# Kernel tuning notes

Hardware: AMD Instinct MI355X
Metric: run time of the kernel (lower is better)

Reference implementation:

```python
import jax, jax.numpy as jnp
import numpy as np

DIM = 1024
ATT_DIM = 1024
NUM_HEADS = 16
HEAD_DIM = ATT_DIM // NUM_HEADS


def setup_inputs() -> dict:
    key = jax.random.key(0)
    ks = jax.random.split(key, 13)
    s = lambda fan_in: 1.0 / np.sqrt(fan_in)
    bsz, n = 8, 1024
    x = jax.random.normal(ks[0], (bsz, n, DIM), dtype=jnp.float32)
    # Linear weights stored as [in, out] (apply via x @ W + b)
    Wq = jax.random.uniform(ks[1], (DIM, ATT_DIM), minval=-s(DIM), maxval=s(DIM))
    bq = jax.random.uniform(ks[2], (ATT_DIM,), minval=-s(DIM), maxval=s(DIM))
    Wk = jax.random.uniform(ks[3], (DIM, ATT_DIM), minval=-s(DIM), maxval=s(DIM))
    bk = jax.random.uniform(ks[4], (ATT_DIM,), minval=-s(DIM), maxval=s(DIM))
    Wv = jax.random.uniform(ks[5], (DIM, ATT_DIM), minval=-s(DIM), maxval=s(DIM))
    bv = jax.random.uniform(ks[6], (ATT_DIM,), minval=-s(DIM), maxval=s(DIM))
    Win = jax.random.uniform(ks[7], (DIM, HEAD_DIM), minval=-s(DIM), maxval=s(DIM))
    bin_ = jax.random.uniform(ks[8], (HEAD_DIM,), minval=-s(DIM), maxval=s(DIM))
    d_in1 = HEAD_DIM * (NUM_HEADS + 1)
    W1 = jax.random.uniform(ks[9], (d_in1, 2 * DIM), minval=-s(d_in1), maxval=s(d_in1))
    b1 = jax.random.uniform(ks[10], (2 * DIM,), minval=-s(d_in1), maxval=s(d_in1))
    W2 = jax.random.uniform(ks[11], (2 * DIM, DIM), minval=-s(2 * DIM), maxval=s(2 * DIM))
    b2 = jax.random.uniform(ks[12], (DIM,), minval=-s(2 * DIM), maxval=s(2 * DIM))
    return {"x": x, "Wq": Wq, "bq": bq, "Wk": Wk, "bk": bk, "Wv": Wv, "bv": bv,
            "Win": Win, "bin_": bin_, "W1": W1, "b1": b1, "W2": W2, "b2": b2}


def reference(x, Wq, bq, Wk, bk, Wv, bv, Win, bin_, W1, b1, W2, b2):
    bsz, n, _ = x.shape
    scaling = HEAD_DIM ** (-0.5)
    # [b, n, h, d]
    q = (x @ Wq + bq).reshape(bsz, n, NUM_HEADS, HEAD_DIM) * scaling
    k = (x @ Wk + bk).reshape(bsz, n, NUM_HEADS, HEAD_DIM)
    v = (x @ Wv + bv).reshape(bsz, n, NUM_HEADS, HEAD_DIM)
    # scores [b, h, n, n]
    score = jnp.einsum('bihd,bjhd->bhij', q, k)
    diag = jnp.eye(n, dtype=bool)  # self positions masked with -inf
    score = jnp.where(diag[None, None], -jnp.inf, score)
    attn = jax.nn.softmax(score, axis=-1)
    out = jnp.einsum('bhij,bjhd->bihd', attn, v).reshape(bsz, n, NUM_HEADS * HEAD_DIM)
    in_ = (x @ Win + bin_)  # [b, n, head_dim]
    out = jnp.concatenate([out, in_], axis=-1)
    h = jax.nn.relu(out @ W1 + b1)
    return h @ W2 + b2
```

## Files before the change

kernel.cpp:

```cpp
#include <hip/hip_runtime.h>

typedef __bf16 bf16;
typedef __attribute__((ext_vector_type(8))) __bf16 bf16x8;
typedef __attribute__((ext_vector_type(4))) __bf16 bf16x4;
typedef __attribute__((ext_vector_type(4))) short short4_t;
typedef __attribute__((ext_vector_type(4))) float floatx4;

typedef const void __attribute__((address_space(1)))* gas1p;
typedef void __attribute__((address_space(3)))* las3p;

#define LOG2E 1.44269504088896340736f

static constexpr int D_MODEL = 1024;
static constexpr int N_HEADS = 16;
static constexpr int HDIM    = 64;
static constexpr int BSZ     = 8;
static constexpr int SEQ     = 1024;
static constexpr int ROWS    = BSZ * SEQ;
static constexpr int FF_IN   = 1088;
static constexpr int FF_HID  = 2048;
static constexpr int QKV_LD  = 3072;

__device__ __forceinline__ floatx4 mfma_bf16(bf16x8 a, bf16x8 b, floatx4 c) {
  return __builtin_amdgcn_mfma_f32_16x16x32_bf16(a, b, c, 0, 0, 0);
}

__device__ __forceinline__ floatx4 mfma16(bf16x4 a, bf16x4 b, floatx4 c) {
#if __has_builtin(__builtin_amdgcn_mfma_f32_16x16x16_bf16)
  return __builtin_amdgcn_mfma_f32_16x16x16_bf16(a, b, c, 0, 0, 0);
#else
  return __builtin_amdgcn_mfma_f32_16x16x16bf16_1k(
      __builtin_bit_cast(short4_t, a), __builtin_bit_cast(short4_t, b), c, 0, 0, 0);
#endif
}

__device__ __forceinline__ float fast_exp2(float x) {
#if __has_builtin(__builtin_amdgcn_exp2f)
  return __builtin_amdgcn_exp2f(x);
#else
  return exp2f(x);
#endif
}

__device__ __forceinline__ float flex_load(const void* src, size_t idx, int isbf) {
  return isbf ? (float)((const bf16*)src)[idx] : ((const float*)src)[idx];
}

struct TransJobs {
  const void* src[6];
  bf16* dst[6];
  int R[6], C[6];
  int tiles_x[6];
  int tile_base[7];
  float scale[6];
};

static constexpr int NBX = (ROWS * D_MODEL) / 2048;
static constexpr int NBB = 25;

__global__ __launch_bounds__(256)
void prep_all_kernel(const void* __restrict__ xsrc, bf16* __restrict__ xdst,
                     const void* bq, const void* bk, const void* bv,
                     const void* bin, const void* b1, const void* b2,
                     float* __restrict__ biasf, TransJobs J,
                     int* __restrict__ flagOut) {
  __shared__ float tile[32][33];
  __shared__ int cnt;
  if (threadIdx.x == 0) cnt = 0;
  __syncthreads();
  {
    const unsigned v = ((const unsigned*)xsrc)[(size_t)threadIdx.x * 997 + 13];
    const unsigned bb = (v >> 8) & 0x7F;
    if (bb >= 0x3B && bb <= 0x41) atomicAdd(&cnt, 1);
  }
  __syncthreads();
  const int isbf = (cnt > 128) ? 1 : 0;
  const int bid = blockIdx.x;
  if (bid == NBX && threadIdx.x == 0) *flagOut = isbf;

  if (bid < NBX) {
    const size_t i = ((size_t)bid * 256 + threadIdx.x) * 8;
    bf16x8 o;
    if (isbf) {
      o = *reinterpret_cast<const bf16x8*>((const bf16*)xsrc + i);
    } else {
      const float4 f0 = *reinterpret_cast<const float4*>((const float*)xsrc + i);
      const float4 f1 = *reinterpret_cast<const float4*>((const float*)xsrc + i + 4);
      o[0] = (bf16)f0.x; o[1] = (bf16)f0.y; o[2] = (bf16)f0.z; o[3] = (bf16)f0.w;
      o[4] = (bf16)f1.x; o[5] = (bf16)f1.y; o[6] = (bf16)f1.z; o[7] = (bf16)f1.w;
    }
    *reinterpret_cast<bf16x8*>(xdst + i) = o;
    return;
  }
  if (bid < NBX + NBB) {
    const int i = (bid - NBX) * 256 + threadIdx.x;
    if (i < 1024)      biasf[i] = flex_load(bq, i, isbf) * (0.125f * LOG2E);
    else if (i < 2048) biasf[i] = flex_load(bk, i - 1024, isbf);
    else if (i < 3072) biasf[i] = flex_load(bv, i - 2048, isbf);
    else if (i < 3136) biasf[i] = flex_load(bin, i - 3072, isbf);
    else if (i < 5184) biasf[i] = flex_load(b1, i - 3136, isbf);
    else if (i < 6208) biasf[i] = flex_load(b2, i - 5184, isbf);
    return;
  }
  const int tb = bid - (NBX + NBB);
  int j = 0;
#pragma unroll
  for (int t = 1; t < 6; t++) j += (tb >= J.tile_base[t]) ? 1 : 0;
  const int t = tb - J.tile_base[j];
  const int c0 = (t % J.tiles_x[j]) * 32, r0 = (t / J.tiles_x[j]) * 32;
  const void* src = J.src[j];
  bf16* dst = J.dst[j];
  const int R = J.R[j], C = J.C[j];
  const float scale = J.scale[j];
  const int tx = threadIdx.x & 31, ty = threadIdx.x >> 5;
  for (int i = ty; i < 32; i += 8)
    tile[i][tx] = flex_load(src, (size_t)(r0 + i) * C + (c0 + tx), isbf);
  __syncthreads();
  for (int i = ty; i < 32; i += 8)
    dst[(size_t)(c0 + i) * R + (r0 + tx)] = (bf16)(tile[tx][i] * scale);
}

template <int BN, bool DO_RELU, bool OUT_FLEX, bool V_TRANS>
__global__ __launch_bounds__(256)
void gemm_bt(const bf16* __restrict__ A, const bf16* __restrict__ BT,
             const float* __restrict__ bias,
             void* __restrict__ Cv, int N, int K, int ldc,
             bf16* __restrict__ C2, int ldc2, int nsplit, int nvalid,
             int gy, bf16* __restrict__ vt_out,
             const int* __restrict__ flag) {
  constexpr int BM = 128, BK = 64;
  constexpr int TCN = BN / 32;
  constexpr int ACH = (BM * BK) / (256 * 8);
  constexpr int BCH = (BN * BK) / (256 * 8);
  __shared__ __align__(16) char smem_raw[(BM * BK + BN * BK) * 2];
  bf16* As = (bf16*)smem_raw;
  bf16* Bs = As + BM * BK;
  const int tid = threadIdx.x;
  const int wave = tid >> 6, lane = tid & 63;
  const int quad = lane >> 4, lo = lane & 15;
  const int wm = wave >> 1, wn = wave & 1;

  int m0, n0;
  if (gy == 0) {
    m0 = blockIdx.x * BM;
    n0 = blockIdx.y * BN;
  } else {
    const int nwg = gridDim.x;
    const int bid = blockIdx.x;
    const int sid = (bid & 7) * (nwg >> 3) + (bid >> 3);
    const int P = gy << 3;
    const int g = sid / P, r2 = sid - g * P;
    m0 = (g * 8 + (r2 & 7)) * BM;
    n0 = (r2 >> 3) * BN;
  }

  floatx4 acc[4][TCN];
#pragma unroll
  for (int i = 0; i < 4; i++)
#pragma unroll
    for (int j = 0; j < TCN; j++) acc[i][j] = floatx4{0.f, 0.f, 0.f, 0.f};

  for (int kb = 0; kb < K; kb += BK) {
#pragma unroll
    for (int u = 0; u < ACH; u++) {
      const int c = u * 256 + tid;
      const int row = c >> 3, col = c & 7;
      const int gcol = col ^ (row & 7);
      const bf16* gp = A + (size_t)(m0 + row) * K + kb + gcol * 8;
      __builtin_amdgcn_global_load_lds((gas1p)gp, (las3p)(As + c * 8), 16, 0, 0);
    }
#pragma unroll
    for (int u = 0; u < BCH; u++) {
      const int c = u * 256 + tid;
      const int row = c >> 3, col = c & 7;
      const int gcol = col ^ (row & 7);
      const bf16* gp = BT + (size_t)(n0 + row) * K + kb + gcol * 8;
      __builtin_amdgcn_global_load_lds((gas1p)gp, (las3p)(Bs + c * 8), 16, 0, 0);
    }
    __syncthreads();
#pragma unroll
    for (int kk = 0; kk < 2; kk++) {
      bf16x8 af[4], bfr[TCN];
#pragma unroll
      for (int tr = 0; tr < 4; tr++) {
        const int row = wm * 64 + tr * 16 + lo;
        const int cc = (kk * 4 + quad) ^ (lo & 7);
        af[tr] = *reinterpret_cast<const bf16x8*>(As + row * BK + cc * 8);
      }
#pragma unroll
      for (int tc = 0; tc < TCN; tc++) {
        const int row = wn * (BN / 2) + tc * 16 + lo;
        const int cc = (kk * 4 + quad) ^ (lo & 7);
        bfr[tc] = *reinterpret_cast<const bf16x8*>(Bs + row * BK + cc * 8);
      }
#pragma unroll
      for (int tr = 0; tr < 4; tr++)
#pragma unroll
        for (int tc = 0; tc < TCN; tc++)
          acc[tr][tc] = mfma_bf16(af[tr], bfr[tc], acc[tr][tc]);
    }
    __syncthreads();
  }

  if (V_TRANS && n0 >= 2048 && n0 < 3072) {
    const int h = ((n0 - 2048) >> 6) + wn;
    const int b = m0 >> 10;
    const int ibase = (m0 & 1023) + wm * 64;
    bf16* L = ((bf16*)smem_raw) + wave * 4096;
#pragma unroll
    for (int tc = 0; tc < TCN; tc++) {
      const int d = tc * 16 + lo;
      const float bval = bias[n0 + wn * 64 + d];
#pragma unroll
      for (int tr = 0; tr < 4; tr++) {
        const int iin = tr * 16 + quad * 4;
        bf16x4 p;
#pragma unroll
        for (int rr = 0; rr < 4; rr++) p[rr] = (bf16)(acc[tr][tc][rr] + bval);
        *reinterpret_cast<bf16x4*>(L + d * 64 + (iin ^ ((d & 7) << 3))) = p;
      }
    }
    asm volatile("s_waitcnt lgkmcnt(0)" ::: "memory");
    bf16* dst = vt_out + (size_t)(b * 16 + h) * (HDIM * SEQ) + ibase;
#pragma unroll
    for (int w8 = 0; w8 < 8; w8++) {
      const int dp = w8 * 8 + (lane >> 3);
      const int ip = (lane & 7) * 8;
      const bf16x8 v = *reinterpret_cast<const bf16x8*>(
          L + dp * 64 + (ip ^ ((dp & 7) << 3)));
      *reinterpret_cast<bf16x8*>(dst + (size_t)dp * SEQ + ip) = v;
    }
    return;
  }

  const int isbf = OUT_FLEX ? *flag : 1;
#pragma unroll
  for (int tc = 0; tc < TCN; tc++) {
    const int col = n0 + wn * (BN / 2) + tc * 16 + lo;
    const float bval = bias[col];
    if (col < nsplit) {
#pragma unroll
      for (int tr = 0; tr < 4; tr++) {
        const int rbase = m0 + wm * 64 + tr * 16 + quad * 4;
#pragma unroll
        for (int rr = 0; rr < 4; rr++) {
          float v = acc[tr][tc][rr] + bval;
          if (DO_RELU) v = fmaxf(v, 0.f);
          const size_t idx = (size_t)(rbase + rr) * ldc + col;
          if (!OUT_FLEX || isbf) ((bf16*)Cv)[idx] = (bf16)v;
          else                   ((float*)Cv)[idx] = v;
        }
      }
    } else if (col < nvalid) {
#pragma unroll
      for (int tr = 0; tr < 4; tr++) {
        const int rbase = m0 + wm * 64 + tr * 16 + quad * 4;
#pragma unroll
        for (int rr = 0; rr < 4; rr++) {
          float v = acc[tr][tc][rr] + bval;
          if (DO_RELU) v = fmaxf(v, 0.f);
          C2[(size_t)(rbase + rr) * ldc2 + (col - nsplit)] = (bf16)v;
        }
      }
    }
  }
}

__global__ __launch_bounds__(256)
void attn_kernel(const bf16* __restrict__ QKV, const bf16* __restrict__ Vt,
                 bf16* __restrict__ Cc) {
  __shared__ bf16 Ks[64 * 64];
  __shared__ bf16 Vs[64 * 64];
  const int bid = blockIdx.x;
  const int xcd = bid & 7, g = bid >> 3;
  const int ib = g & 15, bh = (g >> 4) * 8 + xcd;
  const int b = bh >> 4, h = bh & 15;
  const int i0 = ib * 64;
  const int tid = threadIdx.x, wave = tid >> 6, lane = tid & 63;
  const int quad = lane >> 4, lo = lane & 15;
  const int iw = i0 + wave * 16;
  const bf16* qptr = QKV + (size_t)b * SEQ * QKV_LD + h * HDIM;
  const bf16* kptr = QKV + (size_t)b * SEQ * QKV_LD + 1024 + h * HDIM;
  const bf16* vptr = Vt + (size_t)bh * HDIM * SEQ;

  const int c0 = tid, c1 = 256 + tid;
  const int row0 = c0 >> 3, gcol0 = (c0 & 7) ^ (row0 & 7);
  const int row1 = c1 >> 3, gcol1 = (c1 & 7) ^ (row1 & 7);

  bf16x8 qf[2];
#pragma unroll
  for (int kf = 0; kf < 2; kf++)
    qf[kf] = *reinterpret_cast<const bf16x8*>(
        qptr + (size_t)(iw + lo) * QKV_LD + kf * 32 + quad * 8);

  floatx4 oacc[4];
  float lrow = 0.f;
#pragma unroll
  for (int dt = 0; dt < 4; dt++) oacc[dt] = floatx4{0.f, 0.f, 0.f, 0.f};

  bf16x8 kreg0 = *reinterpret_cast<const bf16x8*>(
      kptr + (size_t)row0 * QKV_LD + gcol0 * 8);
  bf16x8 kreg1 = *reinterpret_cast<const bf16x8*>(
      kptr + (size_t)row1 * QKV_LD + gcol1 * 8);
  bf16x8 vreg0 = *reinterpret_cast<const bf16x8*>(
      vptr + (size_t)row0 * SEQ + gcol0 * 8);
  bf16x8 vreg1 = *reinterpret_cast<const bf16x8*>(
      vptr + (size_t)row1 * SEQ + gcol1 * 8);

  for (int jb = 0; jb < SEQ / 64; jb++) {
    const int j0 = jb * 64;
    __syncthreads();
    *reinterpret_cast<bf16x8*>(Ks + c0 * 8) = kreg0;
    *reinterpret_cast<bf16x8*>(Ks + c1 * 8) = kreg1;
    *reinterpret_cast<bf16x8*>(Vs + c0 * 8) = vreg0;
    *reinterpret_cast<bf16x8*>(Vs + c1 * 8) = vreg1;
    __syncthreads();
    if (jb + 1 < SEQ / 64) {
      const int jn = j0 + 64;
      kreg0 = *reinterpret_cast<const bf16x8*>(
          kptr + (size_t)(jn + row0) * QKV_LD + gcol0 * 8);
      kreg1 = *reinterpret_cast<const bf16x8*>(
          kptr + (size_t)(jn + row1) * QKV_LD + gcol1 * 8);
      vreg0 = *reinterpret_cast<const bf16x8*>(
          vptr + (size_t)row0 * SEQ + jn + gcol0 * 8);
      vreg1 = *reinterpret_cast<const bf16x8*>(
          vptr + (size_t)row1 * SEQ + jn + gcol1 * 8);
    }

    floatx4 sacc[4];
#pragma unroll
    for (int mt = 0; mt < 4; mt++) sacc[mt] = floatx4{0.f, 0.f, 0.f, 0.f};
    __builtin_amdgcn_s_setprio(1);
#pragma unroll
    for (int mt = 0; mt < 4; mt++) {
      const int r = mt * 16 + lo;
      const int cc0 = quad ^ (lo & 7);
      const int cc1 = (4 + quad) ^ (lo & 7);
      const bf16x8 k0 = *reinterpret_cast<const bf16x8*>(Ks + r * 64 + cc0 * 8);
      const bf16x8 k1 = *reinterpret_cast<const bf16x8*>(Ks + r * 64 + cc1 * 8);
      sacc[mt] = mfma_bf16(k0, qf[0], sacc[mt]);
      sacc[mt] = mfma_bf16(k1, qf[1], sacc[mt]);
    }
    __builtin_amdgcn_s_setprio(0);

    if (j0 == i0) {
      const int ig = iw + lo;
#pragma unroll
      for (int mt = 0; mt < 4; mt++)
#pragma unroll
        for (int r = 0; r < 4; r++)
          if (j0 + mt * 16 + quad * 4 + r == ig) sacc[mt][r] = -1e30f;
    }

    bf16x4 pfrag[4];
    {
      float s0 = 0.f, s1 = 0.f;
#pragma unroll
      for (int mt = 0; mt < 4; mt++) {
        bf16x4 pk;
#pragma unroll
        for (int r = 0; r < 4; r++) {
          const float p = fast_exp2(sacc[mt][r]);
          if (mt & 1) s1 += p; else s0 += p;
          pk[r] = (bf16)p;
        }
        pfrag[mt] = pk;
      }
      float s = s0 + s1;
      s += __shfl_xor(s, 16);
      s += __shfl_xor(s, 32);
      lrow += s;
    }

    __builtin_amdgcn_s_setprio(1);
#pragma unroll
    for (int dt = 0; dt < 4; dt++) {
      const int r = dt * 16 + lo;
#pragma unroll
      for (int kt = 0; kt < 4; kt++) {
        const int gch = kt * 2 + (quad >> 1);
        const int cc = gch ^ (lo & 7);
        const bf16x4 vf = *reinterpret_cast<const bf16x4*>(
            Vs + r * 64 + cc * 8 + (quad & 1) * 4);
        oacc[dt] = mfma16(vf, pfrag[kt], oacc[dt]);
      }
    }
    __builtin_amdgcn_s_setprio(0);
  }

  {
    const int ig = iw + lo;
    const float inv = 1.0f / lrow;
    bf16* cb = Cc + ((size_t)b * SEQ + ig) * FF_IN + h * HDIM;
#pragma unroll
    for (int dt = 0; dt < 4; dt++) {
      bf16x4 o;
#pragma unroll
      for (int r = 0; r < 4; r++) o[r] = (bf16)(oacc[dt][r] * inv);
      *reinterpret_cast<bf16x4*>(cb + dt * 16 + quad * 4) = o;
    }
  }
}

extern "C" void kernel_launch(void* const* d_in, const int* in_sizes, int n_in,
                              void* d_out, int out_size, void* d_ws, size_t ws_size,
                              hipStream_t stream) {
  (void)in_sizes; (void)n_in; (void)out_size; (void)ws_size;
  const void* x   = d_in[0];
  const void* Wq  = d_in[1];
  const void* bq  = d_in[2];
  const void* Wk  = d_in[3];
  const void* bk  = d_in[4];
  const void* Wv  = d_in[5];
  const void* bv  = d_in[6];
  const void* Win = d_in[7];
  const void* bin = d_in[8];
  const void* W1  = d_in[9];
  const void* b1  = d_in[10];
  const void* W2  = d_in[11];
  const void* b2  = d_in[12];

  size_t off = 0;
  char* wsb = (char*)d_ws;
  auto alloc = [&](size_t bytes) {
    void* p = (void*)(wsb + off);
    off += (bytes + 255) & ~(size_t)255;
    return p;
  };
  int*   flag  = (int*)alloc(4);
  bf16*  xbf   = (bf16*)alloc((size_t)ROWS * D_MODEL * 2);
  bf16*  WqkvT = (bf16*)alloc((size_t)3200 * 1024 * 2);
  bf16*  W1T   = (bf16*)alloc((size_t)FF_HID * FF_IN * 2);
  bf16*  W2T   = (bf16*)alloc((size_t)D_MODEL * FF_HID * 2);
  float* biasf = (float*)alloc(6208 * 4);
  bf16*  qkv   = (bf16*)alloc((size_t)ROWS * QKV_LD * 2);
  bf16*  vtb   = (bf16*)alloc((size_t)ROWS * D_MODEL * 2);
  bf16*  cbuf  = (bf16*)alloc((size_t)ROWS * FF_IN * 2);
  bf16*  hbuf  = (bf16*)alloc((size_t)ROWS * FF_HID * 2);
  float* b1f   = biasf + 3136;
  float* b2f   = biasf + 5184;

  const dim3 blk(256);

  TransJobs J;
  J.src[0] = Wq;  J.dst[0] = WqkvT;                        J.R[0] = 1024; J.C[0] = 1024; J.scale[0] = 0.125f * LOG2E;
  J.src[1] = Wk;  J.dst[1] = WqkvT + (size_t)1024 * 1024;  J.R[1] = 1024; J.C[1] = 1024; J.scale[1] = 1.0f;
  J.src[2] = Wv;  J.dst[2] = WqkvT + (size_t)2048 * 1024;  J.R[2] = 1024; J.C[2] = 1024; J.scale[2] = 1.0f;
  J.src[3] = Win; J.dst[3] = WqkvT + (size_t)3072 * 1024;  J.R[3] = 1024; J.C[3] = 64;   J.scale[3] = 1.0f;
  J.src[4] = W1;  J.dst[4] = W1T;                          J.R[4] = 1088; J.C[4] = 2048; J.scale[4] = 1.0f;
  J.src[5] = W2;  J.dst[5] = W2T;                          J.R[5] = 2048; J.C[5] = 1024; J.scale[5] = 1.0f;
  int base = 0;
  for (int j = 0; j < 6; j++) {
    J.tiles_x[j] = J.C[j] / 32;
    J.tile_base[j] = base;
    base += (J.R[j] / 32) * (J.C[j] / 32);
  }
  J.tile_base[6] = base;

  prep_all_kernel<<<dim3(NBX + NBB + base), blk, 0, stream>>>(
      x, xbf, bq, bk, bv, bin, b1, b2, biasf, J, flag);

  gemm_bt<128, false, false, true><<<dim3(1600), blk, 0, stream>>>(
      xbf, WqkvT, biasf, qkv, 3200, 1024, QKV_LD,
      cbuf + 1024, FF_IN, 3072, 3136, 25, vtb, nullptr);

  attn_kernel<<<dim3(2048), blk, 0, stream>>>(qkv, vtb, cbuf);

  gemm_bt<128, true, false, false><<<dim3(64, 16), blk, 0, stream>>>(
      cbuf, W1T, b1f, hbuf, FF_HID, FF_IN, FF_HID,
      nullptr, 0, FF_HID, FF_HID, 0, nullptr, nullptr);
  gemm_bt<128, false, true, false><<<dim3(64, 8), blk, 0, stream>>>(
      hbuf, W2T, b2f, d_out, D_MODEL, FF_HID, D_MODEL,
      nullptr, 0, D_MODEL, D_MODEL, 0, nullptr, flag);
}
```

Baseline: 380.1 us.

## Add triple-buffered 256x128 QKV GEMM with direct-to-LDS loads

```diff
diff --git a/kernel.cpp b/kernel.cpp
--- a/kernel.cpp
+++ b/kernel.cpp
@@ -118,6 +118,146 @@
   __syncthreads();
   for (int i = ty; i < 32; i += 8)
     dst[(size_t)(c0 + i) * R + (r0 + tx)] = (bf16)(tile[tx][i] * scale);
+}
+
+__global__ __launch_bounds__(512)
+void gemm_qkv_pipe(const bf16* __restrict__ A, const bf16* __restrict__ BT,
+                   const float* __restrict__ bias, bf16* __restrict__ Cq,
+                   bf16* __restrict__ C2, bf16* __restrict__ vt_out) {
+  constexpr int BM = 256, BN = 128, BK = 64, KDIM = 1024, NT = KDIM / BK;
+  __shared__ __align__(16) bf16 As[3][BM * BK];
+  __shared__ __align__(16) bf16 Bs[3][BN * BK];
+  const int tid = threadIdx.x;
+  const int wave = tid >> 6, lane = tid & 63;
+  const int quad = lane >> 4, lo = lane & 15;
+  const int wm = wave >> 1, wn = wave & 1;
+
+  const int bid = blockIdx.x;
+  const int sid = (bid & 7) * 100 + (bid >> 3);
+  const int g = sid / 200, r2 = sid - g * 200;
+  const int m0 = (g * 8 + (r2 & 7)) * BM;
+  const int n0 = (r2 >> 3) * BN;
+
+  auto stage = [&](int t, int cb) {
+    const size_t kb = (size_t)t * BK;
+#pragma unroll
+    for (int u = 0; u < 4; u++) {
+      const int c = u * 512 + tid;
+      const int row = c >> 3;
+      const int gcol = (c & 7) ^ (row & 7);
+      __builtin_amdgcn_global_load_lds(
+          (gas1p)(A + (size_t)(m0 + row) * KDIM + kb + gcol * 8),
+          (las3p)(&As[cb][c * 8]), 16, 0, 0);
+    }
+#pragma unroll
+    for (int u = 0; u < 2; u++) {
+      const int c = u * 512 + tid;
+      const int row = c >> 3;
+      const int gcol = (c & 7) ^ (row & 7);
+      __builtin_amdgcn_global_load_lds(
+          (gas1p)(BT + (size_t)(n0 + row) * KDIM + kb + gcol * 8),
+          (las3p)(&Bs[cb][c * 8]), 16, 0, 0);
+    }
+  };
+
+  floatx4 acc[4][4];
+#pragma unroll
+  for (int i = 0; i < 4; i++)
+#pragma unroll
+    for (int j = 0; j < 4; j++) acc[i][j] = floatx4{0.f, 0.f, 0.f, 0.f};
+
+  stage(0, 0);
+  stage(1, 1);
+  asm volatile("s_waitcnt vmcnt(6)" ::: "memory");
+  asm volatile("s_barrier" ::: "memory");
+
+  for (int t = 0; t < NT; ++t) {
+    const int cb = t % 3;
+    if (t + 2 < NT) stage(t + 2, (t + 2) % 3);
+    const bf16* Asc = As[cb];
+    const bf16* Bsc = Bs[cb];
+#pragma unroll
+    for (int kk = 0; kk < 2; kk++) {
+      bf16x8 af[4], bfr[4];
+#pragma unroll
+      for (int tr = 0; tr < 4; tr++) {
+        const int row = wm * 64 + tr * 16 + lo;
+        const int cc = (kk * 4 + quad) ^ (lo & 7);
+        af[tr] = *reinterpret_cast<const bf16x8*>(Asc + row * BK + cc * 8);
+      }
+#pragma unroll
+      for (int tc = 0; tc < 4; tc++) {
+        const int row = wn * 64 + tc * 16 + lo;
+        const int cc = (kk * 4 + quad) ^ (lo & 7);
+        bfr[tc] = *reinterpret_cast<const bf16x8*>(Bsc + row * BK + cc * 8);
+      }
+      __builtin_amdgcn_s_setprio(1);
+#pragma unroll
+      for (int tr = 0; tr < 4; tr++)
+#pragma unroll
+        for (int tc = 0; tc < 4; tc++)
+          acc[tr][tc] = mfma_bf16(af[tr], bfr[tc], acc[tr][tc]);
+      __builtin_amdgcn_s_setprio(0);
+    }
+    if (t + 2 < NT)      asm volatile("s_waitcnt vmcnt(6)" ::: "memory");
+    else if (t + 1 < NT) asm volatile("s_waitcnt vmcnt(0)" ::: "memory");
+    asm volatile("s_barrier" ::: "memory");
+  }
+
+  if (n0 >= 2048 && n0 < 3072) {
+    const int h = ((n0 - 2048) >> 6) + wn;
+    const int b = m0 >> 10;
+    const int ibase = (m0 & 1023) + wm * 64;
+    bf16* L = &As[0][0] + wave * 4096;
+#pragma unroll
+    for (int tc = 0; tc < 4; tc++) {
+      const int d = tc * 16 + lo;
+      const float bval = bias[n0 + wn * 64 + d];
+#pragma unroll
+      for (int tr = 0; tr < 4; tr++) {
+        const int iin = tr * 16 + quad * 4;
+        bf16x4 p;
+#pragma unroll
+        for (int rr = 0; rr < 4; rr++) p[rr] = (bf16)(acc[tr][tc][rr] + bval);
+        *reinterpret_cast<bf16x4*>(L + d * 64 + (iin ^ ((d & 7) << 3))) = p;
+      }
+    }
+    asm volatile("s_waitcnt lgkmcnt(0)" ::: "memory");
+    bf16* dst = vt_out + (size_t)(b * 16 + h) * (HDIM * SEQ) + ibase;
+#pragma unroll
+    for (int w8 = 0; w8 < 8; w8++) {
+      const int dp = w8 * 8 + (lane >> 3);
+      const int ip = (lane & 7) * 8;
+      const bf16x8 v = *reinterpret_cast<const bf16x8*>(
+          L + dp * 64 + (ip ^ ((dp & 7) << 3)));
+      *reinterpret_cast<bf16x8*>(dst + (size_t)dp * SEQ + ip) = v;
+    }
+    return;
+  }
+
+#pragma unroll
+  for (int tc = 0; tc < 4; tc++) {
+    const int col = n0 + wn * 64 + tc * 16 + lo;
+    const float bval = bias[col];
+    if (col < 3072) {
+#pragma unroll
+      for (int tr = 0; tr < 4; tr++) {
+        const int rbase = m0 + wm * 64 + tr * 16 + quad * 4;
+#pragma unroll
+        for (int rr = 0; rr < 4; rr++)
+          Cq[(size_t)(rbase + rr) * QKV_LD + col] = (bf16)(acc[tr][tc][rr] + bval);
+      }
+    } else if (col < 3136) {
+#pragma unroll
+      for (int tr = 0; tr < 4; tr++) {
+        const int rbase = m0 + wm * 64 + tr * 16 + quad * 4;
+#pragma unroll
+        for (int rr = 0; rr < 4; rr++)
+          C2[(size_t)(rbase + rr) * FF_IN + (col - 3072)] =
+              (bf16)(acc[tr][tc][rr] + bval);
+      }
+    }
+  }
 }
 
 template <int BN, bool DO_RELU, bool OUT_FLEX, bool V_TRANS>
@@ -460,9 +600,8 @@
   prep_all_kernel<<<dim3(NBX + NBB + base), blk, 0, stream>>>(
       x, xbf, bq, bk, bv, bin, b1, b2, biasf, J, flag);
 
-  gemm_bt<128, false, false, true><<<dim3(1600), blk, 0, stream>>>(
-      xbf, WqkvT, biasf, qkv, 3200, 1024, QKV_LD,
-      cbuf + 1024, FF_IN, 3072, 3136, 25, vtb, nullptr);
+  gemm_qkv_pipe<<<dim3(800), dim3(512), 0, stream>>>(
+      xbf, WqkvT, biasf, qkv, cbuf + 1024, vtb);
 
   attn_kernel<<<dim3(2048), blk, 0, stream>>>(qkv, vtb, cbuf);
 
```

Measured after the change: 384.6 us. No clear change (+1.2%).
